# Kernel optimization log

Measured on AMD Instinct MI355X. Metric: run time of the kernel, lower is better.

The kernel has to match this reference:

```python
import math
import jax, jax.numpy as jnp
import numpy as np


def fwht(x):
    """Fast Walsh-Hadamard transform on the last dim (power of 2), orthonormal."""
    orig_shape = x.shape
    d = orig_shape[-1]
    h = 1
    while h < d:  # log2(d) stages, fixed at trace time
        x = x.reshape(*orig_shape[:-1], -1, 2 * h)
        left = x[..., :h]
        right = x[..., h:]
        x = jnp.concatenate([left + right, left - right], axis=-1)
        x = x.reshape(orig_shape)
        h *= 2
    return x * jnp.asarray(1.0 / math.sqrt(d), dtype=x.dtype)


def setup_inputs() -> dict:
    key = jax.random.key(0)
    k_x, k_s = jax.random.split(key)
    B, D = 16384, 4096  # padded_dim == dim == 4096 (already power of 2)
    x = jax.random.normal(k_x, (B, D), dtype=jnp.float32)
    # random +/-1 signs, mirroring torch.randint(0,2,(D,))*2-1
    signs = jnp.where(jax.random.bernoulli(k_s, 0.5, (D,)), 1.0, -1.0).astype(jnp.float32)
    return {"x": x, "signs": signs}


def reference(x, signs):
    # RandomizedHadamardTransform.forward: sign flip then normalized FWHT.
    # dim == padded_dim here, so no zero-padding branch is taken.
    return fwht(x * signs)
```

## Files before the change

kernel.cpp:

```cpp
#include <hip/hip_runtime.h>
#include <hip/hip_bf16.h>

namespace {

constexpr int D = 4096;
constexpr int NT = 256;

__device__ __forceinline__ int swz(int i) {
    return i ^ (((i >> 8) & 1) << 4) ^ (((i >> 9) & 1) << 3) ^ (((i >> 5) & 1) << 2);
}

__device__ __forceinline__ void fwht16(float v[16]) {
#pragma unroll
    for (int h = 1; h < 16; h <<= 1) {
#pragma unroll
        for (int g = 0; g < 16; g += (h << 1)) {
#pragma unroll
            for (int j = 0; j < h; ++j) {
                const float a = v[g + j];
                const float b = v[g + j + h];
                v[g + j] = a + b;
                v[g + j + h] = a - b;
            }
        }
    }
}

__global__ __launch_bounds__(NT) void rht_kernel(const float* __restrict__ x,
                                                 const float* __restrict__ signs,
                                                 float* __restrict__ out) {
    __shared__ float lds[D];
    const int t = threadIdx.x;
    const size_t row = blockIdx.x;
    const float* __restrict__ xr = x + row * (size_t)D;
    float* __restrict__ outr = out + row * (size_t)D;

    float v[16];

    {
        const float4* __restrict__ x4 = reinterpret_cast<const float4*>(xr) + (t << 2);
        const float4* __restrict__ s4 = reinterpret_cast<const float4*>(signs) + (t << 2);
#pragma unroll
        for (int q = 0; q < 4; ++q) {
            const float4 a = x4[q];
            const float4 s = s4[q];
            v[4 * q + 0] = a.x * s.x;
            v[4 * q + 1] = a.y * s.y;
            v[4 * q + 2] = a.z * s.z;
            v[4 * q + 3] = a.w * s.w;
        }
    }
    fwht16(v);
#pragma unroll
    for (int q = 0; q < 4; ++q) {
        *reinterpret_cast<float4*>(&lds[swz((t << 4) + (q << 2))]) =
            make_float4(v[4 * q], v[4 * q + 1], v[4 * q + 2], v[4 * q + 3]);
    }
    __syncthreads();

    {
        const int b2 = ((t >> 4) << 8) + (t & 15);
#pragma unroll
        for (int k = 0; k < 16; ++k) v[k] = lds[swz(b2 + (k << 4))];
        fwht16(v);
#pragma unroll
        for (int k = 0; k < 16; ++k) lds[swz(b2 + (k << 4))] = v[k];
    }
    __syncthreads();

    {
#pragma unroll
        for (int k = 0; k < 16; ++k) v[k] = lds[swz((k << 8) + t)];
        fwht16(v);
#pragma unroll
        for (int k = 0; k < 16; ++k) lds[swz((k << 8) + t)] = v[k];
    }
    __syncthreads();

#pragma unroll
    for (int m = 0; m < 4; ++m) {
        float4 w = *reinterpret_cast<const float4*>(&lds[swz((t << 2) + (m << 10))]);
        w.x *= 0.015625f;
        w.y *= 0.015625f;
        w.z *= 0.015625f;
        w.w *= 0.015625f;
        *reinterpret_cast<float4*>(&outr[(t << 2) + (m << 10)]) = w;
    }
}

}

extern "C" void kernel_launch(void* const* d_in, const int* in_sizes, int n_in,
                              void* d_out, int out_size, void* d_ws, size_t ws_size,
                              hipStream_t stream) {
    const float* x = (const float*)d_in[0];
    const float* signs = (const float*)d_in[1];
    float* out = (float*)d_out;
    const int B = in_sizes[0] / D;
    rht_kernel<<<dim3(B), dim3(NT), 0, stream>>>(x, signs, out);
}
```

Measured before the change: 96.05 us.

## Process eight rows per block with register prefetch of the next row

Each block now loops over eight rows instead of one. It loads the signs once and prefetches the next row's input into registers while the current row runs through the LDS transform stages. This is meant to hide global load latency and amortize block launch and sign loads. In exchange the grid shrinks to 2048 blocks, an extra barrier is added per row, and register pressure rises, which may lower occupancy and the memory parallelism gained from many resident blocks.

```diff
diff --git a/kernel.cpp b/kernel.cpp
--- a/kernel.cpp
+++ b/kernel.cpp
@@ -5,6 +5,7 @@
 
 constexpr int D = 4096;
 constexpr int NT = 256;
+constexpr int ROWS = 8;
 
 __device__ __forceinline__ int swz(int i) {
     return i ^ (((i >> 8) & 1) << 4) ^ (((i >> 9) & 1) << 3) ^ (((i >> 5) & 1) << 2);
@@ -28,63 +29,92 @@
 
 __global__ __launch_bounds__(NT) void rht_kernel(const float* __restrict__ x,
                                                  const float* __restrict__ signs,
-                                                 float* __restrict__ out) {
+                                                 float* __restrict__ out,
+                                                 int nrows) {
     __shared__ float lds[D];
     const int t = threadIdx.x;
-    const size_t row = blockIdx.x;
-    const float* __restrict__ xr = x + row * (size_t)D;
-    float* __restrict__ outr = out + row * (size_t)D;
+    const int row0 = blockIdx.x * ROWS;
+    if (row0 >= nrows) return;
+    const int nr = min(ROWS, nrows - row0);
 
-    float v[16];
-
+    float sv[16];
     {
-        const float4* __restrict__ x4 = reinterpret_cast<const float4*>(xr) + (t << 2);
         const float4* __restrict__ s4 = reinterpret_cast<const float4*>(signs) + (t << 2);
 #pragma unroll
         for (int q = 0; q < 4; ++q) {
-            const float4 a = x4[q];
             const float4 s = s4[q];
-            v[4 * q + 0] = a.x * s.x;
-            v[4 * q + 1] = a.y * s.y;
-            v[4 * q + 2] = a.z * s.z;
-            v[4 * q + 3] = a.w * s.w;
+            sv[4 * q + 0] = s.x;
+            sv[4 * q + 1] = s.y;
+            sv[4 * q + 2] = s.z;
+            sv[4 * q + 3] = s.w;
         }
     }
-    fwht16(v);
+
+    float4 nxt[4];
+    {
+        const float4* __restrict__ x4 =
+            reinterpret_cast<const float4*>(x + (size_t)row0 * D) + (t << 2);
 #pragma unroll
-    for (int q = 0; q < 4; ++q) {
-        *reinterpret_cast<float4*>(&lds[swz((t << 4) + (q << 2))]) =
-            make_float4(v[4 * q], v[4 * q + 1], v[4 * q + 2], v[4 * q + 3]);
+        for (int q = 0; q < 4; ++q) nxt[q] = x4[q];
     }
-    __syncthreads();
 
-    {
-        const int b2 = ((t >> 4) << 8) + (t & 15);
+#pragma unroll 1
+    for (int r = 0; r < nr; ++r) {
+        float* __restrict__ outr = out + (size_t)(row0 + r) * D;
+
+        float v[16];
 #pragma unroll
-        for (int k = 0; k < 16; ++k) v[k] = lds[swz(b2 + (k << 4))];
+        for (int q = 0; q < 4; ++q) {
+            v[4 * q + 0] = nxt[q].x * sv[4 * q + 0];
+            v[4 * q + 1] = nxt[q].y * sv[4 * q + 1];
+            v[4 * q + 2] = nxt[q].z * sv[4 * q + 2];
+            v[4 * q + 3] = nxt[q].w * sv[4 * q + 3];
+        }
+
+        if (r + 1 < nr) {
+            const float4* __restrict__ x4 =
+                reinterpret_cast<const float4*>(x + (size_t)(row0 + r + 1) * D) + (t << 2);
+#pragma unroll
+            for (int q = 0; q < 4; ++q) nxt[q] = x4[q];
+        }
+
         fwht16(v);
 #pragma unroll
-        for (int k = 0; k < 16; ++k) lds[swz(b2 + (k << 4))] = v[k];
-    }
-    __syncthreads();
+        for (int q = 0; q < 4; ++q) {
+            *reinterpret_cast<float4*>(&lds[swz((t << 4) + (q << 2))]) =
+                make_float4(v[4 * q], v[4 * q + 1], v[4 * q + 2], v[4 * q + 3]);
+        }
+        __syncthreads();
 
-    {
+        {
+            const int b2 = ((t >> 4) << 8) + (t & 15);
 #pragma unroll
-        for (int k = 0; k < 16; ++k) v[k] = lds[swz((k << 8) + t)];
-        fwht16(v);
+            for (int k = 0; k < 16; ++k) v[k] = lds[swz(b2 + (k << 4))];
+            fwht16(v);
 #pragma unroll
-        for (int k = 0; k < 16; ++k) lds[swz((k << 8) + t)] = v[k];
-    }
-    __syncthreads();
+            for (int k = 0; k < 16; ++k) lds[swz(b2 + (k << 4))] = v[k];
+        }
+        __syncthreads();
+
+        {
+#pragma unroll
+            for (int k = 0; k < 16; ++k) v[k] = lds[swz((k << 8) + t)];
+            fwht16(v);
+#pragma unroll
+            for (int k = 0; k < 16; ++k) lds[swz((k << 8) + t)] = v[k];
+        }
+        __syncthreads();
 
 #pragma unroll
-    for (int m = 0; m < 4; ++m) {
-        float4 w = *reinterpret_cast<const float4*>(&lds[swz((t << 2) + (m << 10))]);
-        w.x *= 0.015625f;
-        w.y *= 0.015625f;
-        w.z *= 0.015625f;
-        w.w *= 0.015625f;
-        *reinterpret_cast<float4*>(&outr[(t << 2) + (m << 10)]) = w;
+        for (int m = 0; m < 4; ++m) {
+            float4 w = *reinterpret_cast<const float4*>(&lds[swz((t << 2) + (m << 10))]);
+            w.x *= 0.015625f;
+            w.y *= 0.015625f;
+            w.z *= 0.015625f;
+            w.w *= 0.015625f;
+            *reinterpret_cast<float4*>(&outr[(t << 2) + (m << 10)]) = w;
+        }
+        __syncthreads();
     }
 }
 
@@ -97,5 +127,6 @@
     const float* signs = (const float*)d_in[1];
     float* out = (float*)d_out;
     const int B = in_sizes[0] / D;
-    rht_kernel<<<dim3(B), dim3(NT), 0, stream>>>(x, signs, out);
+    const int grid = (B + ROWS - 1) / ROWS;
+    rht_kernel<<<dim3(grid), dim3(NT), 0, stream>>>(x, signs, out, B);
 }
```

Measured after the change: 112.7 us. +17.3%, slower.
